# Performance work log

Measured on AMD Instinct MI355X. Metric: run time of the kernel, lower is better.

The kernel has to match this reference:

```python
import jax, jax.numpy as jnp
import numpy as np

MAX_POINTS = 2048  # config['object_points']


def setup_inputs() -> dict:
    key = jax.random.key(0)
    k1, k2 = jax.random.split(key)
    B, N, C = 64, 131072, 4
    point_cloud = jax.random.normal(k1, (B, N, C), dtype=jnp.float32)
    logits = jax.random.normal(k2, (B, 2, N), dtype=jnp.float32)
    return {"point_cloud": point_cloud, "logits": logits}


def reference(point_cloud, logits):
    """JAX translation of point_cloud_masking.

    point_cloud: (B, N, C) with xyz in channels 0:3
    logits:      (B, 2, N)
    Returns (object_point_cloud (B, M, 3), mask_xyz_mean (B, 3)).
    """
    M = MAX_POINTS
    B, N, _ = point_cloud.shape
    dtype = point_cloud.dtype

    mask = logits[:, 0, :] < logits[:, 1, :]                  # (B, N) bool
    maskf = mask.astype(dtype)
    count_f = jnp.sum(maskf, axis=1)                          # (B,)
    xyz = point_cloud[..., :3]                                # (B, N, 3)
    mask_xyz_mean = jnp.sum(maskf[..., None] * xyz, axis=1) / jnp.maximum(count_f, 1.0)[:, None]  # (B,3)
    centered = xyz - mask_xyz_mean[:, None, :]                # (B, N, 3)

    # Stable argsort puts masked-point indices first, preserving order (like torch.where).
    order = jnp.argsort(1 - maskf, axis=1, stable=True)       # (B, N) int
    cnt = count_f.astype(jnp.int32)                           # (B,)

    # Resample to fixed M points (with replacement), matching torch.randint semantics:
    #   cnt >  M: all M indices random in [0, cnt)
    #   cnt <  M: first cnt identity, remaining random in [0, cnt)
    #   cnt == M: identity
    ksel = jax.random.key(42)
    rand = jax.random.randint(ksel, (B, M), 0, jnp.maximum(cnt, 1)[:, None])
    j = jnp.arange(M, dtype=jnp.int32)[None, :]               # (1, M)
    keep = (j < cnt[:, None]) & (cnt[:, None] <= M)
    sel = jnp.where(keep, j, rand)                            # (B, M) positions into sorted order
    idx = jnp.take_along_axis(order, sel, axis=1)             # (B, M) original point indices
    obj = jnp.take_along_axis(centered, idx[..., None], axis=1)  # (B, M, 3)

    # Empty-mask fallback: ones * batch_index (matches torch branch).
    empty = (cnt == 0)[:, None, None]
    batch_ids = jnp.arange(B, dtype=dtype)[:, None, None]
    obj = jnp.where(empty, jnp.ones_like(obj) * batch_ids, obj)
    return obj, mask_xyz_mean
```

## Files before the change

kernel.cpp:

```cpp
#include <hip/hip_runtime.h>
#include <stdint.h>

#define BATCH 64
#define NPTS  131072
#define MPTS  2048
#define CHUNK 1024
#define CPB   (NPTS / CHUNK)
#define WORDS_PB (NPTS / 64)

struct U2 { uint32_t a, b; };

__host__ __device__ constexpr U2 tf2x32(uint32_t k0, uint32_t k1, uint32_t x0, uint32_t x1) {
  uint32_t ks0 = k0, ks1 = k1, ks2 = k0 ^ k1 ^ 0x1BD11BDAu;
  x0 += ks0; x1 += ks1;
  const int rotA[4] = {13, 15, 26, 6};
  const int rotB[4] = {17, 29, 16, 24};
  for (int r = 0; r < 4; ++r) { x0 += x1; x1 = (x1 << rotA[r]) | (x1 >> (32 - rotA[r])); x1 ^= x0; }
  x0 += ks1; x1 += ks2 + 1u;
  for (int r = 0; r < 4; ++r) { x0 += x1; x1 = (x1 << rotB[r]) | (x1 >> (32 - rotB[r])); x1 ^= x0; }
  x0 += ks2; x1 += ks0 + 2u;
  for (int r = 0; r < 4; ++r) { x0 += x1; x1 = (x1 << rotA[r]) | (x1 >> (32 - rotA[r])); x1 ^= x0; }
  x0 += ks0; x1 += ks1 + 3u;
  for (int r = 0; r < 4; ++r) { x0 += x1; x1 = (x1 << rotB[r]) | (x1 >> (32 - rotB[r])); x1 ^= x0; }
  x0 += ks1; x1 += ks2 + 4u;
  for (int r = 0; r < 4; ++r) { x0 += x1; x1 = (x1 << rotA[r]) | (x1 >> (32 - rotA[r])); x1 ^= x0; }
  x0 += ks2; x1 += ks0 + 5u;
  return U2{x0, x1};
}

__global__ __launch_bounds__(256) void pass1_kernel(
    const float4* __restrict__ pc, const float4* __restrict__ lg4,
    float* __restrict__ sums, unsigned long long* __restrict__ maskWords) {
  int blk = blockIdx.x;
  int b = blk >> 7;
  int c = blk & (CPB - 1);
  int t = threadIdx.x;

  size_t lbase = (size_t)b * (2 * NPTS / 4) + (size_t)c * (CHUNK / 4) + t;
  float4 a  = lg4[lbase];
  float4 bb = lg4[lbase + NPTS / 4];
  size_t pbase = (size_t)b * NPTS + (size_t)c * CHUNK + 4 * t;
  float4 p0 = pc[pbase + 0];
  float4 p1 = pc[pbase + 1];
  float4 p2 = pc[pbase + 2];
  float4 p3 = pc[pbase + 3];

  bool m0 = a.x < bb.x, m1 = a.y < bb.y, m2 = a.z < bb.z, m3 = a.w < bb.w;
  unsigned nib = (unsigned)m0 | ((unsigned)m1 << 1) | ((unsigned)m2 << 2) | ((unsigned)m3 << 3);

  __shared__ unsigned char sNib[256];
  sNib[t] = (unsigned char)nib;
  __syncthreads();
  if (t < 16) {
    const uint32_t* sN32 = (const uint32_t*)sNib;
    unsigned long long w = 0ull;
#pragma unroll
    for (int q = 0; q < 4; ++q) {
      uint32_t u = sN32[t * 4 + q];
      w |= (unsigned long long)( u        & 0x0Fu) << (q * 16 + 0);
      w |= (unsigned long long)((u >> 8)  & 0x0Fu) << (q * 16 + 4);
      w |= (unsigned long long)((u >> 16) & 0x0Fu) << (q * 16 + 8);
      w |= (unsigned long long)((u >> 24) & 0x0Fu) << (q * 16 + 12);
    }
    maskWords[(size_t)b * WORDS_PB + c * 16 + t] = w;
  }

  float sx = (m0 ? p0.x : 0.f) + (m1 ? p1.x : 0.f) + (m2 ? p2.x : 0.f) + (m3 ? p3.x : 0.f);
  float sy = (m0 ? p0.y : 0.f) + (m1 ? p1.y : 0.f) + (m2 ? p2.y : 0.f) + (m3 ? p3.y : 0.f);
  float sz = (m0 ? p0.z : 0.f) + (m1 ? p1.z : 0.f) + (m2 ? p2.z : 0.f) + (m3 ? p3.z : 0.f);

  for (int o = 32; o; o >>= 1) {
    sx += __shfl_down(sx, o, 64);
    sy += __shfl_down(sy, o, 64);
    sz += __shfl_down(sz, o, 64);
  }
  __shared__ float ssx[4], ssy[4], ssz[4];
  int wave = t >> 6;
  if ((t & 63) == 0) { ssx[wave] = sx; ssy[wave] = sy; ssz[wave] = sz; }
  __syncthreads();
  if (t == 0) {
    atomicAdd(&sums[b * 3 + 0], ssx[0] + ssx[1] + ssx[2] + ssx[3]);
    atomicAdd(&sums[b * 3 + 1], ssy[0] + ssy[1] + ssy[2] + ssy[3]);
    atomicAdd(&sums[b * 3 + 2], ssz[0] + ssz[1] + ssz[2] + ssz[3]);
  }
}

__global__ __launch_bounds__(256) void pass2_kernel(
    const unsigned long long* __restrict__ maskWords, const float* __restrict__ sums,
    uint32_t* __restrict__ wordOff, int* __restrict__ cnt,
    float* __restrict__ mean, float* __restrict__ out) {
  int b = blockIdx.x, t = threadIdx.x;
  const unsigned long long* mw = maskWords + (size_t)b * WORDS_PB;
  int base = t * 8;
  int p[8];
  int local = 0;
#pragma unroll
  for (int k = 0; k < 8; ++k) { p[k] = __popcll(mw[base + k]); local += p[k]; }

  __shared__ int s[256];
  s[t] = local;
  __syncthreads();
  for (int off = 1; off < 256; off <<= 1) {
    int add = (t >= off) ? s[t - off] : 0;
    __syncthreads();
    s[t] += add;
    __syncthreads();
  }
  int run = s[t] - local;
  uint32_t* wo = wordOff + (size_t)b * WORDS_PB;
#pragma unroll
  for (int k = 0; k < 8; ++k) { wo[base + k] = (uint32_t)run; run += p[k]; }

  if (t == 255) {
    int ct = run;
    cnt[b] = ct;
    float d  = fmaxf((float)ct, 1.0f);
    float mx = sums[b * 3 + 0] / d;
    float my = sums[b * 3 + 1] / d;
    float mz = sums[b * 3 + 2] / d;
    mean[b * 3 + 0] = mx; mean[b * 3 + 1] = my; mean[b * 3 + 2] = mz;
    float* om = out + (size_t)BATCH * MPTS * 3 + (size_t)b * 3;
    om[0] = mx; om[1] = my; om[2] = mz;
  }
}

__global__ __launch_bounds__(256) void pass3_kernel(
    const float4* __restrict__ pc, const int* __restrict__ cnt,
    const float* __restrict__ mean, const uint32_t* __restrict__ wordOff,
    const unsigned long long* __restrict__ maskWords,
    float* __restrict__ out) {
  int blk = blockIdx.x;
  int b = blk >> 3;
  int t = threadIdx.x;
  int j = (blk & 7) * 256 + t;
  int gid = b * MPTS + j;

  __shared__ uint32_t sOff[WORDS_PB];
  __shared__ float sMean[3];
  __shared__ int sCnt;
  const uint32_t* wo = wordOff + (size_t)b * WORDS_PB;
#pragma unroll
  for (int k = 0; k < 8; ++k) sOff[t + k * 256] = wo[t + k * 256];
  if (t < 3)  sMean[t] = mean[b * 3 + t];
  if (t == 0) sCnt = cnt[b];
  __syncthreads();

  int cb = sCnt;
  float ox, oy, oz;
  if (cb == 0) {
    ox = oy = oz = (float)b;
  } else {
    constexpr U2 K1 = tf2x32(0u, 42u, 0u, 0u);
    constexpr U2 K2 = tf2x32(0u, 42u, 0u, 1u);
    uint32_t span = (uint32_t)cb;
    U2 h = tf2x32(K1.a, K1.b, 0u, (uint32_t)gid);
    U2 l = tf2x32(K2.a, K2.b, 0u, (uint32_t)gid);
    uint32_t hb = h.a ^ h.b;
    uint32_t lb = l.a ^ l.b;
    uint32_t mul = 65536u % span;
    mul = (mul * mul) % span;
    uint32_t off = ((hb % span) * mul + (lb % span)) % span;
    int r = (j < cb && cb <= MPTS) ? j : (int)off;

    int lo = 0;
#pragma unroll
    for (int step = 1024; step; step >>= 1) {
      int nxt = lo + step;
      if (nxt < WORDS_PB && sOff[nxt] <= (uint32_t)r) lo = nxt;
    }
    int rem = r - (int)sOff[lo];
    unsigned long long w = maskWords[(size_t)b * WORDS_PB + lo];

    uint32_t cur = (uint32_t)w;
    int bitbase = 0;
    int c = __popc(cur);
    if (rem >= c) { rem -= c; cur = (uint32_t)(w >> 32); bitbase = 32; }
    c = __popc(cur & 0xFFFFu); if (rem >= c) { rem -= c; cur >>= 16; bitbase += 16; }
    c = __popc(cur & 0xFFu);   if (rem >= c) { rem -= c; cur >>= 8;  bitbase += 8;  }
    c = __popc(cur & 0xFu);    if (rem >= c) { rem -= c; cur >>= 4;  bitbase += 4;  }
    c = __popc(cur & 0x3u);    if (rem >= c) { rem -= c; cur >>= 2;  bitbase += 2;  }
    c = (int)(cur & 1u);       if (rem >= c) {           cur >>= 1;  bitbase += 1;  }
    int idx = lo * 64 + bitbase;

    float4 p = pc[(size_t)b * NPTS + idx];
    ox = p.x - sMean[0]; oy = p.y - sMean[1]; oz = p.z - sMean[2];
  }
  float* o = out + (size_t)gid * 3;
  o[0] = ox; o[1] = oy; o[2] = oz;
}

extern "C" void kernel_launch(void* const* d_in, const int* in_sizes, int n_in,
                              void* d_out, int out_size, void* d_ws, size_t ws_size,
                              hipStream_t stream) {
  const float4* pc  = (const float4*)d_in[0];
  const float4* lg4 = (const float4*)d_in[1];
  float* out = (float*)d_out;

  char* w = (char*)d_ws;
  int*      cnt     = (int*)(w + 0);
  float*    sums    = (float*)(w + 256);
  float*    mean    = (float*)(w + 1024);
  uint32_t* wordOff = (uint32_t*)(w + 4096);
  unsigned long long* maskWords =
      (unsigned long long*)(w + 4096 + 524288);

  hipMemsetAsync(w + 256, 0, 768, stream);

  pass1_kernel<<<BATCH * CPB, 256, 0, stream>>>(pc, lg4, sums, maskWords);
  pass2_kernel<<<BATCH, 256, 0, stream>>>(maskWords, sums, wordOff, cnt, mean, out);
  pass3_kernel<<<(BATCH * MPTS) / 256, 256, 0, stream>>>(pc, cnt, mean, wordOff, maskWords, out);
}
```

Baseline: 286.9 us.

## Coalesce pass1 loads with ballot-built mask words and use a wave-shuffle scan

The first pass now has each thread handle 16 points across 16 fully coalesced iterations, loading scalar logits and one float4 point per step. The 64-bit mask words come straight from a wavefront ballot instead of nibble packing through shared memory. There are four times fewer blocks, so fewer atomics go to the per-batch sums. The prefix sum in pass2 is replaced by a wave-level shuffle scan plus a small cross-wave combine, removing the barrier-heavy shared-memory scan. The cost is that each block does more serial work, so fewer loads may be in flight at once.

```diff
diff --git a/kernel.cpp b/kernel.cpp
--- a/kernel.cpp
+++ b/kernel.cpp
@@ -4,9 +4,9 @@
 #define BATCH 64
 #define NPTS  131072
 #define MPTS  2048
-#define CHUNK 1024
-#define CPB   (NPTS / CHUNK)
 #define WORDS_PB (NPTS / 64)
+#define P1_PPB 4096
+#define P1_BLOCKS (BATCH * NPTS / P1_PPB)
 
 struct U2 { uint32_t a, b; };
 
@@ -29,45 +29,30 @@
 }
 
 __global__ __launch_bounds__(256) void pass1_kernel(
-    const float4* __restrict__ pc, const float4* __restrict__ lg4,
+    const float4* __restrict__ pc, const float* __restrict__ lg,
     float* __restrict__ sums, unsigned long long* __restrict__ maskWords) {
   int blk = blockIdx.x;
-  int b = blk >> 7;
-  int c = blk & (CPB - 1);
   int t = threadIdx.x;
-
-  size_t lbase = (size_t)b * (2 * NPTS / 4) + (size_t)c * (CHUNK / 4) + t;
-  float4 a  = lg4[lbase];
-  float4 bb = lg4[lbase + NPTS / 4];
-  size_t pbase = (size_t)b * NPTS + (size_t)c * CHUNK + 4 * t;
-  float4 p0 = pc[pbase + 0];
-  float4 p1 = pc[pbase + 1];
-  float4 p2 = pc[pbase + 2];
-  float4 p3 = pc[pbase + 3];
-
-  bool m0 = a.x < bb.x, m1 = a.y < bb.y, m2 = a.z < bb.z, m3 = a.w < bb.w;
-  unsigned nib = (unsigned)m0 | ((unsigned)m1 << 1) | ((unsigned)m2 << 2) | ((unsigned)m3 << 3);
-
-  __shared__ unsigned char sNib[256];
-  sNib[t] = (unsigned char)nib;
-  __syncthreads();
-  if (t < 16) {
-    const uint32_t* sN32 = (const uint32_t*)sNib;
-    unsigned long long w = 0ull;
-#pragma unroll
-    for (int q = 0; q < 4; ++q) {
-      uint32_t u = sN32[t * 4 + q];
-      w |= (unsigned long long)( u        & 0x0Fu) << (q * 16 + 0);
-      w |= (unsigned long long)((u >> 8)  & 0x0Fu) << (q * 16 + 4);
-      w |= (unsigned long long)((u >> 16) & 0x0Fu) << (q * 16 + 8);
-      w |= (unsigned long long)((u >> 24) & 0x0Fu) << (q * 16 + 12);
+  size_t pbase = (size_t)blk * P1_PPB;
+  int b = (int)(pbase >> 17);
+  const float* l0g = lg + (size_t)b * NPTS;
+  const float* l1g = lg + (size_t)(b + 1) * NPTS;
+
+  float sx = 0.f, sy = 0.f, sz = 0.f;
+#pragma unroll 2
+  for (int half = 0; half < 2; ++half) {
+#pragma unroll
+    for (int k = 0; k < 8; ++k) {
+      size_t p = pbase + (size_t)(half * 8 + k) * 256 + t;
+      float a0 = l0g[p];
+      float a1 = l1g[p];
+      float4 q = pc[p];
+      bool m = a0 < a1;
+      unsigned long long bal = __ballot(m);
+      if ((t & 63) == 0) maskWords[p >> 6] = bal;
+      if (m) { sx += q.x; sy += q.y; sz += q.z; }
     }
-    maskWords[(size_t)b * WORDS_PB + c * 16 + t] = w;
-  }
-
-  float sx = (m0 ? p0.x : 0.f) + (m1 ? p1.x : 0.f) + (m2 ? p2.x : 0.f) + (m3 ? p3.x : 0.f);
-  float sy = (m0 ? p0.y : 0.f) + (m1 ? p1.y : 0.f) + (m2 ? p2.y : 0.f) + (m3 ? p3.y : 0.f);
-  float sz = (m0 ? p0.z : 0.f) + (m1 ? p1.z : 0.f) + (m2 ? p2.z : 0.f) + (m3 ? p3.z : 0.f);
+  }
 
   for (int o = 32; o; o >>= 1) {
     sx += __shfl_down(sx, o, 64);
@@ -90,6 +75,7 @@
     uint32_t* __restrict__ wordOff, int* __restrict__ cnt,
     float* __restrict__ mean, float* __restrict__ out) {
   int b = blockIdx.x, t = threadIdx.x;
+  int lane = t & 63, wv = t >> 6;
   const unsigned long long* mw = maskWords + (size_t)b * WORDS_PB;
   int base = t * 8;
   int p[8];
@@ -97,22 +83,25 @@
 #pragma unroll
   for (int k = 0; k < 8; ++k) { p[k] = __popcll(mw[base + k]); local += p[k]; }
 
-  __shared__ int s[256];
-  s[t] = local;
+  int x = local;
+#pragma unroll
+  for (int o = 1; o < 64; o <<= 1) {
+    int y = __shfl_up(x, o, 64);
+    if (lane >= o) x += y;
+  }
+  __shared__ int wsum[4];
+  if (lane == 63) wsum[wv] = x;
   __syncthreads();
-  for (int off = 1; off < 256; off <<= 1) {
-    int add = (t >= off) ? s[t - off] : 0;
-    __syncthreads();
-    s[t] += add;
-    __syncthreads();
-  }
-  int run = s[t] - local;
+  int add = 0;
+#pragma unroll
+  for (int u = 0; u < 4; ++u) add += (u < wv) ? wsum[u] : 0;
+  int run = add + x - local;
   uint32_t* wo = wordOff + (size_t)b * WORDS_PB;
 #pragma unroll
   for (int k = 0; k < 8; ++k) { wo[base + k] = (uint32_t)run; run += p[k]; }
 
-  if (t == 255) {
-    int ct = run;
+  if (t == 0) {
+    int ct = wsum[0] + wsum[1] + wsum[2] + wsum[3];
     cnt[b] = ct;
     float d  = fmaxf((float)ct, 1.0f);
     float mx = sums[b * 3 + 0] / d;
@@ -192,21 +181,21 @@
 extern "C" void kernel_launch(void* const* d_in, const int* in_sizes, int n_in,
                               void* d_out, int out_size, void* d_ws, size_t ws_size,
                               hipStream_t stream) {
-  const float4* pc  = (const float4*)d_in[0];
-  const float4* lg4 = (const float4*)d_in[1];
+  const float4* pc = (const float4*)d_in[0];
+  const float*  lg = (const float*)d_in[1];
   float* out = (float*)d_out;
 
   char* w = (char*)d_ws;
-  int*      cnt     = (int*)(w + 0);
-  float*    sums    = (float*)(w + 256);
-  float*    mean    = (float*)(w + 1024);
+  float*    sums    = (float*)(w + 0);
+  int*      cnt     = (int*)(w + 1024);
+  float*    mean    = (float*)(w + 2048);
   uint32_t* wordOff = (uint32_t*)(w + 4096);
   unsigned long long* maskWords =
       (unsigned long long*)(w + 4096 + 524288);
 
-  hipMemsetAsync(w + 256, 0, 768, stream);
-
-  pass1_kernel<<<BATCH * CPB, 256, 0, stream>>>(pc, lg4, sums, maskWords);
+  hipMemsetAsync(sums, 0, 768, stream);
+
+  pass1_kernel<<<P1_BLOCKS, 256, 0, stream>>>(pc, lg, sums, maskWords);
   pass2_kernel<<<BATCH, 256, 0, stream>>>(maskWords, sums, wordOff, cnt, mean, out);
   pass3_kernel<<<(BATCH * MPTS) / 256, 256, 0, stream>>>(pc, cnt, mean, wordOff, maskWords, out);
 }
```

Measured after the change: 248.7 us. 1.15x faster.
